# Kernel optimization log

Hardware: AMD Instinct MI355X
Metric: run time of the kernel (lower is better)

Reference implementation:

```python
import jax, jax.numpy as jnp
import numpy as np

FEATURES = 1024
PAGES = 16384
K = 32
BATCH = 8192


def setup_inputs() -> dict:
    key = jax.random.key(0)
    k1, k2, k3 = jax.random.split(key, 3)
    x = jax.random.normal(k1, (BATCH, FEATURES), dtype=jnp.float32)
    # encoder: nn.Linear(features, pages) -> weight [pages, features], bias zero-init
    enc_w = jax.random.normal(k2, (PAGES, FEATURES), dtype=jnp.float32) / np.sqrt(FEATURES)
    enc_b = jnp.zeros((PAGES,), dtype=jnp.float32)
    # decoder: nn.Linear(pages, features, bias=False) -> weight [features, pages]
    # initialized as encoder.weight.T, column-normalized (dim=0)
    dec_w = enc_w.T  # [features, pages]
    dec_w = dec_w / jnp.linalg.norm(dec_w, axis=0, keepdims=True)
    bias = jnp.zeros((FEATURES,), dtype=jnp.float32)
    return {"x": x, "enc_w": enc_w, "enc_b": enc_b, "dec_w": dec_w, "bias": bias}


def reference(x, enc_w, enc_b, dec_w, bias):
    # encode: relu(Linear(x - bias))
    pre = jnp.einsum('bf,pf->bp', x - bias, enc_w) + enc_b  # [B, P]
    acts = jax.nn.relu(pre)
    vals, idx = jax.lax.top_k(acts, K)  # [B, K]
    # scatter topk values into a zero buffer of shape [B, P]
    rows = jnp.arange(acts.shape[0])[:, None]  # [B, 1]
    encoded = jnp.zeros_like(acts).at[rows, idx].set(vals)  # [B, P]
    # decode: Linear(encoded) + bias
    xhat = jnp.einsum('bp,fp->bf', encoded, dec_w) + bias  # [B, F]
    return xhat
```

## Files before the change

kernel.cpp:

```cpp
#include <hip/hip_runtime.h>
#include <math.h>

#define FEATURES 1024
#define PAGES    16384
#define BATCH    8192
#define TOPK     32

#define TAU_SIGMA 2.5f
#define CAP       256
#define DELTA     0.05f
#define BCAP      96

typedef float          f32x4  __attribute__((ext_vector_type(4)));
typedef __bf16         bf16x8 __attribute__((ext_vector_type(8)));
typedef unsigned short u16x8  __attribute__((ext_vector_type(8)));

__device__ __forceinline__ unsigned short f2bf(float f) {
    unsigned u = __float_as_uint(f);
    u += 0x7fff + ((u >> 16) & 1);
    return (unsigned short)(u >> 16);
}
__device__ __forceinline__ float bf2f(unsigned short s) {
    return __uint_as_float(((unsigned)s) << 16);
}

__global__ __launch_bounds__(256)
void k_prep_x(const float* __restrict__ x, const float* __restrict__ bias,
              unsigned short* __restrict__ xb) {
    size_t i = ((size_t)blockIdx.x * 256 + threadIdx.x) * 8;
    int k = (int)(i & (FEATURES - 1));
    float4 a0 = *(const float4*)(x + i);
    float4 a1 = *(const float4*)(x + i + 4);
    float4 b0 = *(const float4*)(bias + k);
    float4 b1 = *(const float4*)(bias + k + 4);
    u16x8 o;
    o[0] = f2bf(a0.x - b0.x); o[1] = f2bf(a0.y - b0.y);
    o[2] = f2bf(a0.z - b0.z); o[3] = f2bf(a0.w - b0.w);
    o[4] = f2bf(a1.x - b1.x); o[5] = f2bf(a1.y - b1.y);
    o[6] = f2bf(a1.z - b1.z); o[7] = f2bf(a1.w - b1.w);
    *(u16x8*)(xb + i) = o;
}

__global__ __launch_bounds__(256)
void k_prep_w(const float* __restrict__ w, unsigned short* __restrict__ wb) {
    size_t i = ((size_t)blockIdx.x * 256 + threadIdx.x) * 8;
    float4 a0 = *(const float4*)(w + i);
    float4 a1 = *(const float4*)(w + i + 4);
    u16x8 o;
    o[0] = f2bf(a0.x); o[1] = f2bf(a0.y); o[2] = f2bf(a0.z); o[3] = f2bf(a0.w);
    o[4] = f2bf(a1.x); o[5] = f2bf(a1.y); o[6] = f2bf(a1.z); o[7] = f2bf(a1.w);
    *(u16x8*)(wb + i) = o;
}

__global__ __launch_bounds__(256)
void k_tau(const float* __restrict__ x, const float* __restrict__ bias,
           float* __restrict__ tau) {
    int row  = blockIdx.x * 4 + (threadIdx.x >> 6);
    int lane = threadIdx.x & 63;
    const float* xr = x + (size_t)row * FEATURES;
    float s = 0.f;
    for (int j = lane; j < FEATURES; j += 64) {
        float v = xr[j] - bias[j];
        s += v * v;
    }
    #pragma unroll
    for (int off = 32; off; off >>= 1) s += __shfl_down(s, off);
    if (lane == 0) tau[row] = TAU_SIGMA * sqrtf(s) * (1.0f / 32.0f);
}

#define GBM 128
#define GBN 128
#define GBK 64
#define NKI (FEATURES / GBK)

__global__ __launch_bounds__(256, 2)
void k_gemm_filter_mfma(const unsigned short* __restrict__ xb,
                        const unsigned short* __restrict__ wb,
                        const float* __restrict__ enc_b,
                        const float* __restrict__ tau,
                        int* __restrict__ cnt, int2* __restrict__ cand) {
    __shared__ __align__(16) unsigned short Alds[2][GBM * GBK];
    __shared__ __align__(16) unsigned short Blds[2][GBN * GBK];

    const int tid  = threadIdx.x;
    const int wave = tid >> 6, lane = tid & 63;
    const int wm = wave >> 1, wn = wave & 1;
    const int lr = lane & 15, lq = lane >> 4;
    const int row0 = blockIdx.x * GBM;
    const int col0 = blockIdx.y * GBN;

    f32x4 acc[4][4];
    #pragma unroll
    for (int i = 0; i < 4; i++)
        #pragma unroll
        for (int j = 0; j < 4; j++) acc[i][j] = (f32x4)0.f;

    size_t aoff[4], boff[4];
    int    lsl[4];
    #pragma unroll
    for (int i = 0; i < 4; i++) {
        int slot = i * 256 + tid;
        int r    = slot >> 3;
        int kq   = (slot & 7) ^ (r & 7);
        aoff[i]  = (size_t)(row0 + r) * FEATURES + kq * 8;
        boff[i]  = (size_t)(col0 + r) * FEATURES + kq * 8;
        lsl[i]   = slot * 8;
    }

#define STAGE(buf, kt)                                                        \
    do {                                                                      \
        _Pragma("unroll")                                                     \
        for (int i_ = 0; i_ < 4; i_++) {                                      \
            __builtin_amdgcn_global_load_lds(                                 \
                (const __attribute__((address_space(1))) void*)(xb + aoff[i_] + (kt)), \
                (__attribute__((address_space(3))) void*)(&Alds[buf][lsl[i_]]), 16, 0, 0); \
            __builtin_amdgcn_global_load_lds(                                 \
                (const __attribute__((address_space(1))) void*)(wb + boff[i_] + (kt)), \
                (__attribute__((address_space(3))) void*)(&Blds[buf][lsl[i_]]), 16, 0, 0); \
        }                                                                     \
    } while (0)

#define COMPUTE(buf)                                                          \
    do {                                                                      \
        _Pragma("unroll")                                                     \
        for (int p_ = 0; p_ < 2; p_++) {                                      \
            u16x8 af[4], bfr[4];                                              \
            _Pragma("unroll")                                                 \
            for (int i_ = 0; i_ < 4; i_++) {                                  \
                int rl = wm * 64 + i_ * 16 + lr;                              \
                int ch = (p_ * 4 + lq) ^ (lr & 7);                            \
                af[i_] = *(const u16x8*)(&Alds[buf][(size_t)rl * GBK + ch * 8]); \
            }                                                                 \
            _Pragma("unroll")                                                 \
            for (int j_ = 0; j_ < 4; j_++) {                                  \
                int rl = wn * 64 + j_ * 16 + lr;                              \
                int ch = (p_ * 4 + lq) ^ (lr & 7);                            \
                bfr[j_] = *(const u16x8*)(&Blds[buf][(size_t)rl * GBK + ch * 8]); \
            }                                                                 \
            _Pragma("unroll")                                                 \
            for (int i_ = 0; i_ < 4; i_++)                                    \
                _Pragma("unroll")                                             \
                for (int j_ = 0; j_ < 4; j_++)                                \
                    acc[i_][j_] = __builtin_amdgcn_mfma_f32_16x16x32_bf16(    \
                        __builtin_bit_cast(bf16x8, af[i_]),                   \
                        __builtin_bit_cast(bf16x8, bfr[j_]),                  \
                        acc[i_][j_], 0, 0, 0);                                \
        }                                                                     \
    } while (0)

    STAGE(0, 0);
    asm volatile("s_waitcnt vmcnt(0)" ::: "memory");
    __builtin_amdgcn_s_barrier();

    #pragma unroll 2
    for (int t = 0; t < NKI; t++) {
        if (t + 1 < NKI) {
            STAGE((t + 1) & 1, (t + 1) * GBK);
            asm volatile("s_waitcnt vmcnt(8)" ::: "memory");
        } else {
            asm volatile("s_waitcnt vmcnt(0)" ::: "memory");
        }
        COMPUTE(t & 1);
        asm volatile("s_waitcnt lgkmcnt(0)" ::: "memory");
        __builtin_amdgcn_s_barrier();
    }
#undef STAGE
#undef COMPUTE

    float eb[4];
    #pragma unroll
    for (int j = 0; j < 4; j++) eb[j] = enc_b[col0 + wn * 64 + j * 16 + lr];
    #pragma unroll
    for (int i = 0; i < 4; i++) {
        int rbase = row0 + wm * 64 + i * 16 + lq * 4;
        float tv[4];
        #pragma unroll
        for (int r = 0; r < 4; r++) tv[r] = tau[rbase + r];
        #pragma unroll
        for (int r = 0; r < 4; r++) {
            int row = rbase + r;
            #pragma unroll
            for (int j = 0; j < 4; j++) {
                float v = acc[i][j][r] + eb[j];
                if (v >= tv[r]) {
                    int pos = atomicAdd(&cnt[row], 1);
                    if (pos < CAP) {
                        int2 e;
                        e.x = col0 + wn * 64 + j * 16 + lr;
                        e.y = __float_as_int(v);
                        cand[(size_t)row * CAP + pos] = e;
                    }
                }
            }
        }
    }
}

__global__ __launch_bounds__(256)
void k_refine2(const float* __restrict__ x, const float* __restrict__ bias,
               const float* __restrict__ enc_w, const float* __restrict__ enc_b,
               const int* __restrict__ cnt, const int2* __restrict__ cand,
               int* __restrict__ topk_p, float* __restrict__ topk_v) {
    int row = blockIdx.x;
    int tid = threadIdx.x;
    __shared__ float  xs[FEATURES];
    __shared__ float  av[CAP];
    __shared__ int    ap[CAP];
    __shared__ float  q;
    __shared__ int    bidx[BCAP];
    __shared__ double bval[BCAP];
    __shared__ int    scnt, bcnt;

    for (int j = tid; j < FEATURES; j += 256)
        xs[j] = x[(size_t)row * FEATURES + j] - bias[j];
    int n = cnt[row];
    if (n > CAP) n = CAP;
    if (tid < n) {
        int2 e = cand[(size_t)row * CAP + tid];
        ap[tid] = e.x;
        av[tid] = __int_as_float(e.y);
    }
    if (tid == 0) { scnt = 0; bcnt = 0; }
    __syncthreads();

    if (n <= TOPK) {
        if (tid < TOPK) {
            topk_p[(size_t)row * TOPK + tid] = (tid < n) ? ap[tid] : 0;
            topk_v[(size_t)row * TOPK + tid] = (tid < n) ? fmaxf(av[tid], 0.f) : 0.f;
        }
        return;
    }

    if (tid < n) {
        float v = av[tid];
        int r = 0;
        for (int j = 0; j < n; j++) {
            float u = av[j];
            r += (u > v) || (u == v && j < tid);
        }
        if (r == TOPK - 1) q = v;
    }
    __syncthreads();
    float qv = q;

    bool sure = (tid < n) && (av[tid] >= qv + DELTA);
    bool bnd  = (tid < n) && (av[tid] >= qv - DELTA) && !sure;
    if (sure) {
        int s = atomicAdd(&scnt, 1);
        topk_p[(size_t)row * TOPK + s] = ap[tid];
        topk_v[(size_t)row * TOPK + s] = fmaxf(av[tid], 0.f);
    }
    if (bnd) {
        int b = atomicAdd(&bcnt, 1);
        if (b < BCAP) bidx[b] = tid;
    }
    __syncthreads();

    int ns = scnt;
    int nb = bcnt < BCAP ? bcnt : BCAP;
    int need = TOPK - ns;

    int wave = tid >> 6, lane = tid & 63;
    for (int c = wave; c < nb; c += 4) {
        const float* wrow = enc_w + (size_t)ap[bidx[c]] * FEATURES;
        double a = 0.0;
        #pragma unroll 4
        for (int j = lane; j < FEATURES; j += 64)
            a += (double)xs[j] * (double)wrow[j];
        #pragma unroll
        for (int off = 32; off; off >>= 1) a += __shfl_down(a, off);
        if (lane == 0) bval[c] = a + (double)enc_b[ap[bidx[c]]];
    }
    __syncthreads();

    if (tid < nb) {
        double v = bval[tid];
        int r = 0;
        for (int j = 0; j < nb; j++) {
            double u = bval[j];
            r += (u > v) || (u == v && j < tid);
        }
        if (r < need) {
            int s = atomicAdd(&scnt, 1);
            double rl = v > 0.0 ? v : 0.0;
            topk_p[(size_t)row * TOPK + s] = ap[bidx[tid]];
            topk_v[(size_t)row * TOPK + s] = (float)rl;
        }
    }
}

__global__ __launch_bounds__(256)
void k_transpose_bf(const float* __restrict__ dec_w, unsigned short* __restrict__ dec_wT) {
    __shared__ float tile[32][33];
    int bx = blockIdx.x;
    int by = blockIdx.y;
    int p0 = bx * 32 + threadIdx.x;
    #pragma unroll
    for (int j = 0; j < 32; j += 8) {
        int f = by * 32 + threadIdx.y + j;
        tile[threadIdx.y + j][threadIdx.x] = dec_w[(size_t)f * PAGES + p0];
    }
    __syncthreads();
    int f = by * 32 + threadIdx.x;
    #pragma unroll
    for (int j = 0; j < 32; j += 8) {
        int p = bx * 32 + threadIdx.y + j;
        dec_wT[(size_t)p * FEATURES + f] = f2bf(tile[threadIdx.x][threadIdx.y + j]);
    }
}

__global__ __launch_bounds__(256)
void k_decode_bf(const unsigned short* __restrict__ dec_wT, const float* __restrict__ bias,
                 const int* __restrict__ topk_p, const float* __restrict__ topk_v,
                 float* __restrict__ out) {
    int row = blockIdx.x;
    int tid = threadIdx.x;
    __shared__ int   ps[TOPK];
    __shared__ float vs[TOPK];
    if (tid < TOPK) {
        ps[tid] = topk_p[(size_t)row * TOPK + tid];
        vs[tid] = topk_v[(size_t)row * TOPK + tid];
    }
    __syncthreads();
    int f = tid * 4;
    float4 acc = *(const float4*)(bias + f);
    #pragma unroll
    for (int k = 0; k < TOPK; k++) {
        ushort4 w = *(const ushort4*)(dec_wT + (size_t)ps[k] * FEATURES + f);
        float v = vs[k];
        acc.x = fmaf(v, bf2f(w.x), acc.x);
        acc.y = fmaf(v, bf2f(w.y), acc.y);
        acc.z = fmaf(v, bf2f(w.z), acc.z);
        acc.w = fmaf(v, bf2f(w.w), acc.w);
    }
    *(float4*)(out + (size_t)row * FEATURES + f) = acc;
}

__global__ __launch_bounds__(256)
void k_decode_direct(const float* __restrict__ dec_w, const float* __restrict__ bias,
                     const int* __restrict__ topk_p, const float* __restrict__ topk_v,
                     float* __restrict__ out) {
    int row = blockIdx.x;
    int tid = threadIdx.x;
    __shared__ int   ps[TOPK];
    __shared__ float vs[TOPK];
    if (tid < TOPK) {
        ps[tid] = topk_p[(size_t)row * TOPK + tid];
        vs[tid] = topk_v[(size_t)row * TOPK + tid];
    }
    __syncthreads();
    for (int f = tid; f < FEATURES; f += 256) {
        float acc = bias[f];
        #pragma unroll
        for (int k = 0; k < TOPK; k++)
            acc = fmaf(vs[k], dec_w[(size_t)f * PAGES + ps[k]], acc);
        out[(size_t)row * FEATURES + f] = acc;
    }
}

extern "C" void kernel_launch(void* const* d_in, const int* in_sizes, int n_in,
                              void* d_out, int out_size, void* d_ws, size_t ws_size,
                              hipStream_t stream) {
    const float* x     = (const float*)d_in[0];
    const float* enc_w = (const float*)d_in[1];
    const float* enc_b = (const float*)d_in[2];
    const float* dec_w = (const float*)d_in[3];
    const float* bias  = (const float*)d_in[4];
    float* out = (float*)d_out;

    const size_t SZ_XB    = (size_t)BATCH * FEATURES * 2;
    const size_t SZ_WB    = (size_t)PAGES * FEATURES * 2;
    const size_t SZ_DECWT = (size_t)PAGES * FEATURES * 2;
    const size_t SZ_TAU   = (size_t)BATCH * sizeof(float);
    const size_t SZ_CNT   = (size_t)BATCH * sizeof(int);
    const size_t SZ_CAND  = (size_t)BATCH * CAP * sizeof(int2);
    const size_t SZ_TKP   = (size_t)BATCH * TOPK * sizeof(int);

    const size_t region0 = SZ_XB + SZ_WB;
    char* ws = (char*)d_ws;
    unsigned short* xb     = (unsigned short*)ws;
    unsigned short* wb     = (unsigned short*)(ws + SZ_XB);
    unsigned short* dec_wT = (unsigned short*)ws;
    float* tau    = (float*)(ws + region0);
    int*   cnt    = (int*)  (ws + region0 + SZ_TAU);
    int2*  cand   = (int2*) (ws + region0 + SZ_TAU + SZ_CNT);
    int*   topk_p = (int*)  (ws + region0 + SZ_TAU + SZ_CNT + SZ_CAND);
    float* topk_v = (float*)(ws + region0 + SZ_TAU + SZ_CNT + SZ_CAND + SZ_TKP);

    const bool useT = ws_size >= region0 + SZ_TAU + SZ_CNT + SZ_CAND + 2 * SZ_TKP
                      && SZ_DECWT <= region0;

    hipMemsetAsync(cnt, 0, SZ_CNT, stream);
    k_prep_x<<<BATCH * FEATURES / 2048, 256, 0, stream>>>(x, bias, xb);
    k_prep_w<<<PAGES * FEATURES / 2048, 256, 0, stream>>>(enc_w, wb);
    k_tau<<<BATCH / 4, 256, 0, stream>>>(x, bias, tau);
    k_gemm_filter_mfma<<<dim3(BATCH / GBM, PAGES / GBN), 256, 0, stream>>>(
        xb, wb, enc_b, tau, cnt, cand);
    k_refine2<<<BATCH, 256, 0, stream>>>(x, bias, enc_w, enc_b, cnt, cand, topk_p, topk_v);
    if (useT) {
        k_transpose_bf<<<dim3(PAGES / 32, FEATURES / 32), dim3(32, 8), 0, stream>>>(dec_w, dec_wT);
        k_decode_bf<<<BATCH, 256, 0, stream>>>(dec_wT, bias, topk_p, topk_v, out);
    } else {
        k_decode_direct<<<BATCH, 256, 0, stream>>>(dec_w, bias, topk_p, topk_v, out);
    }
}
```

Baseline: 788.6 us.

## Enlarge GEMM tile to 256x256 with 8 waves and phased load/MFMA pipeline

The encoder GEMM moves from 128x128 tiles with 4 waves to 256x256 tiles with 8 waves. The K loop is split into four phases per buffer, each issuing half of an A or B stage load while MFMAs run. Barriers and s_setprio wrap the MFMA bursts so waves interleave loads and math. The larger tile cuts global reloads of each operand, at the cost of more LDS (128 KB across double buffers) and more accumulator registers. That may limit occupancy to one block per CU.

New measurement: 771.2 us. 2.2% less time.

```diff
diff --git a/kernel.cpp b/kernel.cpp
--- a/kernel.cpp
+++ b/kernel.cpp
@@ -68,12 +68,13 @@
     if (lane == 0) tau[row] = TAU_SIGMA * sqrtf(s) * (1.0f / 32.0f);
 }
 
-#define GBM 128
-#define GBN 128
+#define GBM 256
+#define GBN 256
 #define GBK 64
-#define NKI (FEATURES / GBK)
-
-__global__ __launch_bounds__(256, 2)
+#define NKT (FEATURES / GBK)
+#define NIT (NKT / 2)
+
+__global__ __launch_bounds__(512, 2)
 void k_gemm_filter_mfma(const unsigned short* __restrict__ xb,
                         const unsigned short* __restrict__ wb,
                         const float* __restrict__ enc_b,
@@ -84,95 +85,137 @@
 
     const int tid  = threadIdx.x;
     const int wave = tid >> 6, lane = tid & 63;
-    const int wm = wave >> 1, wn = wave & 1;
+    const int wm = wave >> 2, wn = wave & 3;
     const int lr = lane & 15, lq = lane >> 4;
     const int row0 = blockIdx.x * GBM;
     const int col0 = blockIdx.y * GBN;
 
-    f32x4 acc[4][4];
-    #pragma unroll
-    for (int i = 0; i < 4; i++)
+    f32x4 acc[8][4];
+    #pragma unroll
+    for (int i = 0; i < 8; i++)
         #pragma unroll
         for (int j = 0; j < 4; j++) acc[i][j] = (f32x4)0.f;
 
-    size_t aoff[4], boff[4];
-    int    lsl[4];
-    #pragma unroll
-    for (int i = 0; i < 4; i++) {
-        int slot = i * 256 + tid;
+    unsigned aoffs[2], boffs[2];
+    int lsl[2];
+    #pragma unroll
+    for (int i = 0; i < 2; i++) {
+        int slot = i * 512 + tid;
         int r    = slot >> 3;
         int kq   = (slot & 7) ^ (r & 7);
-        aoff[i]  = (size_t)(row0 + r) * FEATURES + kq * 8;
-        boff[i]  = (size_t)(col0 + r) * FEATURES + kq * 8;
+        aoffs[i] = (unsigned)(row0 + r) * FEATURES + kq * 8;
+        boffs[i] = (unsigned)(col0 + r) * FEATURES + kq * 8;
         lsl[i]   = slot * 8;
     }
 
-#define STAGE(buf, kt)                                                        \
+#define STAGE_A(buf, h, kt)                                                   \
     do {                                                                      \
         _Pragma("unroll")                                                     \
-        for (int i_ = 0; i_ < 4; i_++) {                                      \
+        for (int i_ = 0; i_ < 2; i_++) {                                      \
             __builtin_amdgcn_global_load_lds(                                 \
-                (const __attribute__((address_space(1))) void*)(xb + aoff[i_] + (kt)), \
-                (__attribute__((address_space(3))) void*)(&Alds[buf][lsl[i_]]), 16, 0, 0); \
-            __builtin_amdgcn_global_load_lds(                                 \
-                (const __attribute__((address_space(1))) void*)(wb + boff[i_] + (kt)), \
-                (__attribute__((address_space(3))) void*)(&Blds[buf][lsl[i_]]), 16, 0, 0); \
+                (const __attribute__((address_space(1))) void*)(              \
+                    xb + aoffs[i_] + (h) * 131072u + (unsigned)(kt) * GBK),   \
+                (__attribute__((address_space(3))) void*)(                    \
+                    &Alds[buf][(h) * 8192 + lsl[i_]]), 16, 0, 0);             \
         }                                                                     \
     } while (0)
 
-#define COMPUTE(buf)                                                          \
+#define STAGE_B(buf, h, kt)                                                   \
     do {                                                                      \
         _Pragma("unroll")                                                     \
-        for (int p_ = 0; p_ < 2; p_++) {                                      \
-            u16x8 af[4], bfr[4];                                              \
+        for (int i_ = 0; i_ < 2; i_++) {                                      \
+            __builtin_amdgcn_global_load_lds(                                 \
+                (const __attribute__((address_space(1))) void*)(              \
+                    wb + boffs[i_] + (h) * 131072u + (unsigned)(kt) * GBK),   \
+                (__attribute__((address_space(3))) void*)(                    \
+                    &Blds[buf][(h) * 8192 + lsl[i_]]), 16, 0, 0);             \
+        }                                                                     \
+    } while (0)
+
+#define VM4 asm volatile("s_waitcnt vmcnt(4)" ::: "memory")
+#define VM0 asm volatile("s_waitcnt vmcnt(0)" ::: "memory")
+
+#define PHASE(cbuf, q, RB, STAGE, VMW)                                        \
+    do {                                                                      \
+        u16x8 af[2][2];                                                       \
+        _Pragma("unroll")                                                     \
+        for (int r_ = 0; r_ < 2; r_++) {                                      \
             _Pragma("unroll")                                                 \
-            for (int i_ = 0; i_ < 4; i_++) {                                  \
-                int rl = wm * 64 + i_ * 16 + lr;                              \
-                int ch = (p_ * 4 + lq) ^ (lr & 7);                            \
-                af[i_] = *(const u16x8*)(&Alds[buf][(size_t)rl * GBK + ch * 8]); \
+            for (int kc_ = 0; kc_ < 2; kc_++) {                               \
+                int rl = wm * 128 + ((q) * 2 + r_) * 16 + lr;                 \
+                int ch = (kc_ * 4 + lq) ^ (lr & 7);                           \
+                af[r_][kc_] = *(const u16x8*)(&Alds[cbuf][rl * GBK + ch * 8]);\
             }                                                                 \
+        }                                                                     \
+        if (RB) {                                                             \
             _Pragma("unroll")                                                 \
             for (int j_ = 0; j_ < 4; j_++) {                                  \
-                int rl = wn * 64 + j_ * 16 + lr;                              \
-                int ch = (p_ * 4 + lq) ^ (lr & 7);                            \
-                bfr[j_] = *(const u16x8*)(&Blds[buf][(size_t)rl * GBK + ch * 8]); \
+                _Pragma("unroll")                                             \
+                for (int kc_ = 0; kc_ < 2; kc_++) {                           \
+                    int rl = wn * 64 + j_ * 16 + lr;                          \
+                    int ch = (kc_ * 4 + lq) ^ (lr & 7);                       \
+                    bfr[j_][kc_] = *(const u16x8*)(&Blds[cbuf][rl * GBK + ch * 8]); \
+                }                                                             \
             }                                                                 \
+        }                                                                     \
+        STAGE                                                                 \
+        VMW                                                                   \
+        __builtin_amdgcn_s_barrier();                                         \
+        asm volatile("s_waitcnt lgkmcnt(0)" ::: "memory");                    \
+        __builtin_amdgcn_s_setprio(1);                                        \
+        _Pragma("unroll")                                                     \
+        for (int r_ = 0; r_ < 2; r_++)                                        \
             _Pragma("unroll")                                                 \
-            for (int i_ = 0; i_ < 4; i_++)                                    \
+            for (int j_ = 0; j_ < 4; j_++)                                    \
                 _Pragma("unroll")                                             \
-                for (int j_ = 0; j_ < 4; j_++)                                \
-                    acc[i_][j_] = __builtin_amdgcn_mfma_f32_16x16x32_bf16(    \
-                        __builtin_bit_cast(bf16x8, af[i_]),                   \
-                        __builtin_bit_cast(bf16x8, bfr[j_]),                  \
-                        acc[i_][j_], 0, 0, 0);                                \
-        }                                                                     \
+                for (int kc_ = 0; kc_ < 2; kc_++)                             \
+                    acc[(q) * 2 + r_][j_] =                                   \
+                        __builtin_amdgcn_mfma_f32_16x16x32_bf16(              \
+                            __builtin_bit_cast(bf16x8, af[r_][kc_]),          \
+                            __builtin_bit_cast(bf16x8, bfr[j_][kc_]),         \
+                            acc[(q) * 2 + r_][j_], 0, 0, 0);                  \
+        __builtin_amdgcn_s_setprio(0);                                        \
+        __builtin_amdgcn_s_barrier();                                         \
     } while (0)
 
-    STAGE(0, 0);
-    asm volatile("s_waitcnt vmcnt(0)" ::: "memory");
+    STAGE_A(0, 0, 0); STAGE_A(0, 1, 0);
+    STAGE_B(0, 0, 0); STAGE_B(0, 1, 0);
+    STAGE_B(1, 0, 1); STAGE_B(1, 1, 1);
+    VM4;
     __builtin_amdgcn_s_barrier();
 
-    #pragma unroll 2
-    for (int t = 0; t < NKI; t++) {
-        if (t + 1 < NKI) {
-            STAGE((t + 1) & 1, (t + 1) * GBK);
-            asm volatile("s_waitcnt vmcnt(8)" ::: "memory");
-        } else {
-            asm volatile("s_waitcnt vmcnt(0)" ::: "memory");
-        }
-        COMPUTE(t & 1);
-        asm volatile("s_waitcnt lgkmcnt(0)" ::: "memory");
-        __builtin_amdgcn_s_barrier();
-    }
-#undef STAGE
-#undef COMPUTE
+    u16x8 bfr[4][2];
+    #pragma unroll 1
+    for (int it = 0; it < NIT - 1; ++it) {
+        PHASE(0, 0, 1, STAGE_A(1, 0, 2 * it + 1);, );
+        PHASE(0, 1, 0, STAGE_A(1, 1, 2 * it + 1);, );
+        PHASE(0, 2, 0, STAGE_B(0, 0, 2 * it + 2);, );
+        PHASE(0, 3, 0, STAGE_B(0, 1, 2 * it + 2);, VM4;);
+        PHASE(1, 0, 1, STAGE_A(0, 0, 2 * it + 2);, );
+        PHASE(1, 1, 0, STAGE_A(0, 1, 2 * it + 2);, );
+        PHASE(1, 2, 0, STAGE_B(1, 0, 2 * it + 3);, );
+        PHASE(1, 3, 0, STAGE_B(1, 1, 2 * it + 3);, VM4;);
+    }
+    PHASE(0, 0, 1, STAGE_A(1, 0, NKT - 1);, );
+    PHASE(0, 1, 0, STAGE_A(1, 1, NKT - 1);, );
+    PHASE(0, 2, 0, , );
+    PHASE(0, 3, 0, , VM0;);
+    PHASE(1, 0, 1, , );
+    PHASE(1, 1, 0, , );
+    PHASE(1, 2, 0, , );
+    PHASE(1, 3, 0, , );
+#undef STAGE_A
+#undef STAGE_B
+#undef PHASE
+#undef VM4
+#undef VM0
 
     float eb[4];
     #pragma unroll
     for (int j = 0; j < 4; j++) eb[j] = enc_b[col0 + wn * 64 + j * 16 + lr];
     #pragma unroll
-    for (int i = 0; i < 4; i++) {
-        int rbase = row0 + wm * 64 + i * 16 + lq * 4;
+    for (int i = 0; i < 8; i++) {
+        int rbase = row0 + wm * 128 + i * 16 + lq * 4;
         float tv[4];
         #pragma unroll
         for (int r = 0; r < 4; r++) tv[r] = tau[rbase + r];
@@ -394,7 +437,7 @@
     k_prep_x<<<BATCH * FEATURES / 2048, 256, 0, stream>>>(x, bias, xb);
     k_prep_w<<<PAGES * FEATURES / 2048, 256, 0, stream>>>(enc_w, wb);
     k_tau<<<BATCH / 4, 256, 0, stream>>>(x, bias, tau);
-    k_gemm_filter_mfma<<<dim3(BATCH / GBM, PAGES / GBN), 256, 0, stream>>>(
+    k_gemm_filter_mfma<<<dim3(BATCH / GBM, PAGES / GBN), 512, 0, stream>>>(
         xb, wb, enc_b, tau, cnt, cand);
     k_refine2<<<BATCH, 256, 0, stream>>>(x, bias, enc_w, enc_b, cnt, cand, topk_p, topk_v);
     if (useT) {
```
